# Optimization experiments

Measured on AMD Instinct MI355X. Metric: run time of the kernel, lower is better.

The kernel has to match this reference:

```python
import jax, jax.numpy as jnp
import numpy as np

B, C, LH, LW = 2, 64, 64, 64
KSIZE = 3
HO, WO = LH * 4, LW * 4          # fold output size
HR, WR = HO - KSIZE + 1, WO - KSIZE + 1  # ref spatial size so unfold L == fold L


def setup_inputs() -> dict:
    key = jax.random.key(0)
    k1, k2, k3 = jax.random.split(key, 3)
    lr = jax.random.normal(k1, (B, C, LH, LW), dtype=jnp.float32)
    ref = jax.random.normal(k2, (B, C, HR, WR), dtype=jnp.float32)
    L = HR * WR
    index_map = jax.random.randint(k3, (B, L), 0, L)
    return {"lr": lr, "ref": ref, "index_map": index_map}


def reference(lr, ref, index_map):
    b, c, lh, lw = lr.shape
    k = KSIZE
    ho, wo = lh * 4, lw * 4
    hr, wr = ref.shape[2], ref.shape[3]
    # 'same' padding for ksize=3, stride=1, rate=1 -> reflect pad 1 on each side
    padded = jnp.pad(ref, ((0, 0), (0, 0), (1, 1), (1, 1)), mode='reflect')
    # im2col / unfold, torch channel ordering (C, kh, kw): [B, C, k, k, hr, wr]
    patches = jnp.stack(
        [jnp.stack([padded[:, :, i:i + hr, j:j + wr] for j in range(k)], axis=2)
         for i in range(k)], axis=2)
    patches = patches.reshape(b, c * k * k, hr * wr)  # [B, C*k*k, L]
    # indexed gather along the patch (L) dimension
    idx = jnp.broadcast_to(index_map[:, None, :], patches.shape)
    warped = jnp.take_along_axis(patches, idx, axis=2)
    # col2im / fold with overlap-add to (ho, wo), kernel k, stride 1, pad 0
    hb, wb = ho - k + 1, wo - k + 1  # == hr, wr
    p = warped.reshape(b, c, k, k, hb, wb)
    out = jnp.zeros((b, c, ho, wo), dtype=ref.dtype)
    for i in range(k):
        for j in range(k):
            out = out.at[:, :, i:i + hb, j:j + wb].add(p[:, :, i, j])
    return out
```

## Files before the change

kernel.cpp:

```cpp
#include <hip/hip_runtime.h>
#include <hip/hip_fp16.h>


#define B_   2
#define C_   64
#define HR_  254
#define WR_  254
#define HO_  256
#define WO_  256
#define L_   (HR_ * WR_)
#define PLANE_ (HO_ * WO_ * C_)

__global__ __launch_bounds__(256) void pad_transpose_h2(
    const float* __restrict__ ref, _Float16* __restrict__ P)
{
    __shared__ unsigned short srow[C_][66];

    unsigned bid  = blockIdx.x;
    unsigned b    = bid >> 10;
    unsigned rest = bid & 1023u;
    unsigned py   = rest >> 2;
    unsigned x0   = (rest & 3u) * 64u;
    int ry = (py == 0) ? 1 : ((py == HO_ - 1) ? HR_ - 2 : (int)py - 1);

    const float* rrow = ref + ((size_t)b * C_) * (HR_ * WR_) + (size_t)ry * WR_;
    unsigned tid = threadIdx.x;

    #pragma unroll
    for (unsigned k = 0; k < 16; ++k) {
        unsigned e = k * 256u + tid;
        unsigned c = e >> 6, u = e & 63u;
        unsigned px = x0 + u;
        int rx = (px == 0) ? 1 : ((px == WO_ - 1) ? WR_ - 2 : (int)px - 1);
        float v = rrow[(size_t)c * (HR_ * WR_) + rx];
        _Float16 h = (_Float16)v;
        srow[c][u] = __builtin_bit_cast(unsigned short, h);
    }
    __syncthreads();

    _Float16* prow = P + ((size_t)(b * HO_ + py) * WO_ + x0) * C_;
    #pragma unroll
    for (unsigned it = 0; it < 8; ++it) {
        unsigned u2  = it * 256u + tid;
        unsigned cp  = u2 & 31u;
        unsigned pxl = u2 >> 5;
        unsigned pk = (unsigned)srow[2 * cp][pxl]
                    | ((unsigned)srow[2 * cp + 1][pxl] << 16);
        *reinterpret_cast<unsigned*>(prow + (size_t)pxl * C_ + 2 * cp) = pk;
    }
}

__global__ __launch_bounds__(256) void warp_gather4_kernel(
    const _Float16* __restrict__ P,
    const int*      __restrict__ index_map,
    float*          __restrict__ out)
{
    __shared__ unsigned sbase[3][36];
    __shared__ float    slds[32][65];

    unsigned bid  = blockIdx.x;
    unsigned b    = bid >> 11;
    unsigned rest = bid & 2047u;
    unsigned y    = rest >> 3;
    unsigned x0   = (rest & 7u) * 32u;
    unsigned tid  = threadIdx.x;

    const int* imb = index_map + (size_t)b * L_;
    if (tid < 108) {
        unsigned r    = tid / 36;
        unsigned ccol = tid - r * 36;
        int ly = (int)y - 2 + (int)r;
        int lx = (int)(x0 + ccol) - 2;
        unsigned v = 0xFFFFFFFFu;
        if (ly >= 0 && ly < HR_ && lx >= 0 && lx < WR_) {
            unsigned src = (unsigned)imb[ly * WR_ + lx];
            unsigned sy  = src / WR_;
            unsigned sx  = src - sy * WR_;
            v = (sy * (unsigned)WO_ + sx) * (unsigned)C_;
        }
        sbase[r][ccol] = v;
    }
    __syncthreads();

    unsigned wv   = tid >> 6;
    unsigned lane = tid & 63u;
    unsigned q    = lane >> 3;
    unsigned cg   = lane & 7u;
    unsigned pxl  = wv * 8u + q;
    const _Float16* Pp = P + (size_t)b * PLANE_;

    uint4 raw[9];
    float msk[9];
    #pragma unroll
    for (int k = 0; k < 9; ++k) {
        int i = k / 3, j = k % 3;
        unsigned v = sbase[2 - i][pxl + 2u - (unsigned)j];
        bool valid = (v != 0xFFFFFFFFu);
        unsigned off = (valid ? v : 0u)
                     + (unsigned)((i * WO_ + j) * C_) + cg * 8u;
        msk[k] = valid ? 1.0f : 0.0f;
        raw[k] = *reinterpret_cast<const uint4*>(Pp + off);
    }

    float acc[8] = {0.f, 0.f, 0.f, 0.f, 0.f, 0.f, 0.f, 0.f};
    #pragma unroll
    for (int k = 0; k < 9; ++k) {
        union { uint4 u; _Float16 h[8]; } cv;
        cv.u = raw[k];
        #pragma unroll
        for (int m = 0; m < 8; ++m) {
            acc[m] = fmaf((float)cv.h[m], msk[k], acc[m]);
        }
    }
    *reinterpret_cast<float4*>(&slds[pxl][cg * 8u]) =
        make_float4(acc[0], acc[1], acc[2], acc[3]);
    *reinterpret_cast<float4*>(&slds[pxl][cg * 8u + 4u]) =
        make_float4(acc[4], acc[5], acc[6], acc[7]);
    __syncthreads();

    float* ob = out + ((size_t)b * C_) * (HO_ * WO_) + (size_t)y * WO_ + x0;
    #pragma unroll
    for (unsigned it = 0; it < 8; ++it) {
        unsigned u2 = it * 256u + tid;
        unsigned px = u2 & 31u;
        unsigned ch = u2 >> 5;
        __builtin_nontemporal_store(slds[px][ch],
                                    ob + (size_t)ch * (HO_ * WO_) + px);
    }
}

extern "C" void kernel_launch(void* const* d_in, const int* in_sizes, int n_in,
                              void* d_out, int out_size, void* d_ws, size_t ws_size,
                              hipStream_t stream) {
    const float* ref       = (const float*)d_in[1];
    const int*   index_map = (const int*)d_in[2];
    float*       out       = (float*)d_out;

    _Float16* P = (_Float16*)d_ws;
    pad_transpose_h2<<<dim3(B_ * HO_ * 4), dim3(256), 0, stream>>>(ref, P);
    warp_gather4_kernel<<<dim3(B_ * HO_ * 8), dim3(256), 0, stream>>>(P, index_map, out);
}
```

Baseline: 36.01 us.

## Split padded fp16 image into 16-channel planes and interleave channel groups across blocks

The padded fp16 staging buffer changes from one 64-channel interleaved plane to four 16-channel planes per batch. The gather kernel now handles one channel group over 128 pixels per block, with consecutive blocks covering the four groups so their gathers overlap in L2. Each gathered pixel row is 32 bytes instead of 128, which cuts the footprint of the random gathers. The LDS transpose before the output store is dropped: each lane stores its 8 channels directly, so lanes write consecutive pixels. The cost is four times as many index_map loads and address computations per output pixel, plus nontemporal loads in the pad kernel.

```diff
diff --git a/kernel.cpp b/kernel.cpp
--- a/kernel.cpp
+++ b/kernel.cpp
@@ -9,9 +9,9 @@
 #define HO_  256
 #define WO_  256
 #define L_   (HR_ * WR_)
-#define PLANE_ (HO_ * WO_ * C_)
+#define PPLANE_ ((size_t)HO_ * WO_ * 16)
 
-__global__ __launch_bounds__(256) void pad_transpose_h2(
+__global__ __launch_bounds__(256) void pad_transpose_b16(
     const float* __restrict__ ref, _Float16* __restrict__ P)
 {
     __shared__ unsigned short srow[C_][66];
@@ -32,43 +32,48 @@
         unsigned c = e >> 6, u = e & 63u;
         unsigned px = x0 + u;
         int rx = (px == 0) ? 1 : ((px == WO_ - 1) ? WR_ - 2 : (int)px - 1);
-        float v = rrow[(size_t)c * (HR_ * WR_) + rx];
+        float v = __builtin_nontemporal_load(&rrow[(size_t)c * (HR_ * WR_) + rx]);
         _Float16 h = (_Float16)v;
         srow[c][u] = __builtin_bit_cast(unsigned short, h);
     }
     __syncthreads();
 
-    _Float16* prow = P + ((size_t)(b * HO_ + py) * WO_ + x0) * C_;
     #pragma unroll
     for (unsigned it = 0; it < 8; ++it) {
-        unsigned u2  = it * 256u + tid;
-        unsigned cp  = u2 & 31u;
-        unsigned pxl = u2 >> 5;
-        unsigned pk = (unsigned)srow[2 * cp][pxl]
-                    | ((unsigned)srow[2 * cp + 1][pxl] << 16);
-        *reinterpret_cast<unsigned*>(prow + (size_t)pxl * C_ + 2 * cp) = pk;
+        unsigned w   = it * 256u + tid;
+        unsigned g4  = w >> 9;
+        unsigned rem = w & 511u;
+        unsigned pxl = rem >> 3;
+        unsigned cp  = rem & 7u;
+        unsigned c0  = g4 * 16u + cp * 2u;
+        unsigned pk  = (unsigned)srow[c0][pxl]
+                     | ((unsigned)srow[c0 + 1][pxl] << 16);
+        _Float16* pg = P + ((size_t)(b * 4u + g4) * PPLANE_
+                            + ((size_t)py * WO_ + x0 + pxl) * 16u + cp * 2u);
+        *reinterpret_cast<unsigned*>(pg) = pk;
     }
 }
 
-__global__ __launch_bounds__(256) void warp_gather4_kernel(
+__global__ __launch_bounds__(256) void warp_gather5_kernel(
     const _Float16* __restrict__ P,
     const int*      __restrict__ index_map,
     float*          __restrict__ out)
 {
-    __shared__ unsigned sbase[3][36];
-    __shared__ float    slds[32][65];
+    __shared__ unsigned sbase[3][132];
 
-    unsigned bid  = blockIdx.x;
-    unsigned b    = bid >> 11;
-    unsigned rest = bid & 2047u;
-    unsigned y    = rest >> 3;
-    unsigned x0   = (rest & 7u) * 32u;
-    unsigned tid  = threadIdx.x;
+    unsigned bid   = blockIdx.x;
+    unsigned combo = bid & 7u;
+    unsigned inner = bid >> 3;
+    unsigned b     = combo >> 2;
+    unsigned g4    = combo & 3u;
+    unsigned y     = inner >> 1;
+    unsigned x0    = (inner & 1u) * 128u;
+    unsigned tid   = threadIdx.x;
 
     const int* imb = index_map + (size_t)b * L_;
-    if (tid < 108) {
-        unsigned r    = tid / 36;
-        unsigned ccol = tid - r * 36;
+    for (unsigned e = tid; e < 3 * 130; e += 256) {
+        unsigned r    = e / 130;
+        unsigned ccol = e - r * 130;
         int ly = (int)y - 2 + (int)r;
         int lx = (int)(x0 + ccol) - 2;
         unsigned v = 0xFFFFFFFFu;
@@ -76,7 +81,7 @@
             unsigned src = (unsigned)imb[ly * WR_ + lx];
             unsigned sy  = src / WR_;
             unsigned sx  = src - sy * WR_;
-            v = (sy * (unsigned)WO_ + sx) * (unsigned)C_;
+            v = (sy * (unsigned)WO_ + sx) * 16u;
         }
         sbase[r][ccol] = v;
     }
@@ -84,10 +89,10 @@
 
     unsigned wv   = tid >> 6;
     unsigned lane = tid & 63u;
-    unsigned q    = lane >> 3;
-    unsigned cg   = lane & 7u;
-    unsigned pxl  = wv * 8u + q;
-    const _Float16* Pp = P + (size_t)b * PLANE_;
+    unsigned pq   = lane >> 1;
+    unsigned h    = lane & 1u;
+    unsigned pxl  = wv * 32u + pq;
+    const _Float16* Pp = P + (size_t)combo * PPLANE_;
 
     uint4 raw[9];
     float msk[9];
@@ -97,7 +102,7 @@
         unsigned v = sbase[2 - i][pxl + 2u - (unsigned)j];
         bool valid = (v != 0xFFFFFFFFu);
         unsigned off = (valid ? v : 0u)
-                     + (unsigned)((i * WO_ + j) * C_) + cg * 8u;
+                     + (unsigned)((i * WO_ + j) * 16) + h * 8u;
         msk[k] = valid ? 1.0f : 0.0f;
         raw[k] = *reinterpret_cast<const uint4*>(Pp + off);
     }
@@ -105,27 +110,20 @@
     float acc[8] = {0.f, 0.f, 0.f, 0.f, 0.f, 0.f, 0.f, 0.f};
     #pragma unroll
     for (int k = 0; k < 9; ++k) {
-        union { uint4 u; _Float16 h[8]; } cv;
+        union { uint4 u; _Float16 hh[8]; } cv;
         cv.u = raw[k];
         #pragma unroll
         for (int m = 0; m < 8; ++m) {
-            acc[m] = fmaf((float)cv.h[m], msk[k], acc[m]);
+            acc[m] = fmaf((float)cv.hh[m], msk[k], acc[m]);
         }
     }
-    *reinterpret_cast<float4*>(&slds[pxl][cg * 8u]) =
-        make_float4(acc[0], acc[1], acc[2], acc[3]);
-    *reinterpret_cast<float4*>(&slds[pxl][cg * 8u + 4u]) =
-        make_float4(acc[4], acc[5], acc[6], acc[7]);
-    __syncthreads();
 
     float* ob = out + ((size_t)b * C_) * (HO_ * WO_) + (size_t)y * WO_ + x0;
     #pragma unroll
-    for (unsigned it = 0; it < 8; ++it) {
-        unsigned u2 = it * 256u + tid;
-        unsigned px = u2 & 31u;
-        unsigned ch = u2 >> 5;
-        __builtin_nontemporal_store(slds[px][ch],
-                                    ob + (size_t)ch * (HO_ * WO_) + px);
+    for (int m = 0; m < 8; ++m) {
+        unsigned ch = g4 * 16u + h * 8u + (unsigned)m;
+        __builtin_nontemporal_store(acc[m],
+            ob + (size_t)ch * (HO_ * WO_) + pxl);
     }
 }
 
@@ -137,6 +135,6 @@
     float*       out       = (float*)d_out;
 
     _Float16* P = (_Float16*)d_ws;
-    pad_transpose_h2<<<dim3(B_ * HO_ * 4), dim3(256), 0, stream>>>(ref, P);
-    warp_gather4_kernel<<<dim3(B_ * HO_ * 8), dim3(256), 0, stream>>>(P, index_map, out);
+    pad_transpose_b16<<<dim3(B_ * HO_ * 4), dim3(256), 0, stream>>>(ref, P);
+    warp_gather5_kernel<<<dim3(B_ * HO_ * 8), dim3(256), 0, stream>>>(P, index_map, out);
 }
```

After: 41.54 us. +15.3%, slower.

## Drop LDS transpose in gather kernel, remap blocks, use nontemporal loads

Applied to the files above, without the earlier changes.

The gather kernel now splits channels across wave pairs (16 pixels x 4 channel-groups per wave), so each thread writes its 8 accumulated channels straight to the NCHW output. This removes the shared-memory staging buffer and the second barrier. Block indices are permuted so consecutive workgroups come from different row regions, which changes L2/XCD locality. The pad kernel also uses nontemporal loads for the input. The cost is that each store instruction now writes 16 contiguous floats per channel row instead of full coalesced 32-pixel rows.

```diff
diff --git a/kernel.cpp b/kernel.cpp
--- a/kernel.cpp
+++ b/kernel.cpp
@@ -9,7 +9,7 @@
 #define HO_  256
 #define WO_  256
 #define L_   (HR_ * WR_)
-#define PLANE_ (HO_ * WO_ * C_)
+#define PLANE_ ((size_t)HO_ * WO_ * C_)
 
 __global__ __launch_bounds__(256) void pad_transpose_h2(
     const float* __restrict__ ref, _Float16* __restrict__ P)
@@ -32,7 +32,7 @@
         unsigned c = e >> 6, u = e & 63u;
         unsigned px = x0 + u;
         int rx = (px == 0) ? 1 : ((px == WO_ - 1) ? WR_ - 2 : (int)px - 1);
-        float v = rrow[(size_t)c * (HR_ * WR_) + rx];
+        float v = __builtin_nontemporal_load(&rrow[(size_t)c * (HR_ * WR_) + rx]);
         _Float16 h = (_Float16)v;
         srow[c][u] = __builtin_bit_cast(unsigned short, h);
     }
@@ -50,17 +50,17 @@
     }
 }
 
-__global__ __launch_bounds__(256) void warp_gather4_kernel(
+__global__ __launch_bounds__(256) void warp_gather7_kernel(
     const _Float16* __restrict__ P,
     const int*      __restrict__ index_map,
     float*          __restrict__ out)
 {
     __shared__ unsigned sbase[3][36];
-    __shared__ float    slds[32][65];
 
-    unsigned bid  = blockIdx.x;
-    unsigned b    = bid >> 11;
-    unsigned rest = bid & 2047u;
+    unsigned p  = blockIdx.x;
+    unsigned wg = (p & 7u) * 512u + (p >> 3);
+    unsigned b    = wg >> 11;
+    unsigned rest = wg & 2047u;
     unsigned y    = rest >> 3;
     unsigned x0   = (rest & 7u) * 32u;
     unsigned tid  = threadIdx.x;
@@ -84,9 +84,10 @@
 
     unsigned wv   = tid >> 6;
     unsigned lane = tid & 63u;
-    unsigned q    = lane >> 3;
-    unsigned cg   = lane & 7u;
-    unsigned pxl  = wv * 8u + q;
+    unsigned pq   = lane & 15u;
+    unsigned cg   = lane >> 4;
+    unsigned pxl  = (wv >> 1) * 16u + pq;
+    unsigned chb  = (wv & 1u) * 32u;
     const _Float16* Pp = P + (size_t)b * PLANE_;
 
     uint4 raw[9];
@@ -97,7 +98,7 @@
         unsigned v = sbase[2 - i][pxl + 2u - (unsigned)j];
         bool valid = (v != 0xFFFFFFFFu);
         unsigned off = (valid ? v : 0u)
-                     + (unsigned)((i * WO_ + j) * C_) + cg * 8u;
+                     + (unsigned)((i * WO_ + j) * C_) + chb + cg * 8u;
         msk[k] = valid ? 1.0f : 0.0f;
         raw[k] = *reinterpret_cast<const uint4*>(Pp + off);
     }
@@ -105,27 +106,20 @@
     float acc[8] = {0.f, 0.f, 0.f, 0.f, 0.f, 0.f, 0.f, 0.f};
     #pragma unroll
     for (int k = 0; k < 9; ++k) {
-        union { uint4 u; _Float16 h[8]; } cv;
+        union { uint4 u; _Float16 hh[8]; } cv;
         cv.u = raw[k];
         #pragma unroll
         for (int m = 0; m < 8; ++m) {
-            acc[m] = fmaf((float)cv.h[m], msk[k], acc[m]);
+            acc[m] = fmaf((float)cv.hh[m], msk[k], acc[m]);
         }
     }
-    *reinterpret_cast<float4*>(&slds[pxl][cg * 8u]) =
-        make_float4(acc[0], acc[1], acc[2], acc[3]);
-    *reinterpret_cast<float4*>(&slds[pxl][cg * 8u + 4u]) =
-        make_float4(acc[4], acc[5], acc[6], acc[7]);
-    __syncthreads();
 
     float* ob = out + ((size_t)b * C_) * (HO_ * WO_) + (size_t)y * WO_ + x0;
     #pragma unroll
-    for (unsigned it = 0; it < 8; ++it) {
-        unsigned u2 = it * 256u + tid;
-        unsigned px = u2 & 31u;
-        unsigned ch = u2 >> 5;
-        __builtin_nontemporal_store(slds[px][ch],
-                                    ob + (size_t)ch * (HO_ * WO_) + px);
+    for (int m = 0; m < 8; ++m) {
+        unsigned ch = chb + cg * 8u + (unsigned)m;
+        __builtin_nontemporal_store(acc[m],
+            ob + (size_t)ch * (HO_ * WO_) + pxl);
     }
 }
 
@@ -138,5 +132,5 @@
 
     _Float16* P = (_Float16*)d_ws;
     pad_transpose_h2<<<dim3(B_ * HO_ * 4), dim3(256), 0, stream>>>(ref, P);
-    warp_gather4_kernel<<<dim3(B_ * HO_ * 8), dim3(256), 0, stream>>>(P, index_map, out);
+    warp_gather7_kernel<<<dim3(B_ * HO_ * 8), dim3(256), 0, stream>>>(P, index_map, out);
 }
```

Result: slower. 46.43 us (+28.9%).
